# Optimization experiments

Hardware: AMD Instinct MI355X
Metric: run time of the kernel (lower is better)

## Reference

```python
import jax, jax.numpy as jnp
from jax import lax
import numpy as np

D = 1024      # input_size
H = D // 2    # proj hidden
T = 25        # num_ner_labels
B, S = 64, 512


def setup_inputs() -> dict:
    key = jax.random.key(0)
    ks = jax.random.split(key, 8)
    sc1 = 1.0 / np.sqrt(D)
    sc2 = 1.0 / np.sqrt(H)
    return {
        "encoder_out": jax.random.normal(ks[0], (B, S, D), dtype=jnp.float32),
        "W1": jax.random.uniform(ks[1], (D, H), jnp.float32, -sc1, sc1),
        "b1": jax.random.uniform(ks[2], (H,), jnp.float32, -sc1, sc1),
        "W2": jax.random.uniform(ks[3], (H, T), jnp.float32, -sc2, sc2),
        "b2": jax.random.uniform(ks[4], (T,), jnp.float32, -sc2, sc2),
        "start_trans": jax.random.uniform(ks[5], (T,), jnp.float32, -0.1, 0.1),
        "end_trans": jax.random.uniform(ks[6], (T,), jnp.float32, -0.1, 0.1),
        "trans": jax.random.uniform(ks[7], (T, T), jnp.float32, -0.1, 0.1),
        "ner_labels": jax.random.randint(jax.random.fold_in(key, 1), (B, S), 0, T, dtype=jnp.int64),
        "mask": jnp.ones((B, S), dtype=bool),
    }


def _crf_nll(emissions, start_trans, end_trans, trans, labels, mask):
    # torchcrf negative mean log-likelihood, batch_first
    maskf = mask.astype(emissions.dtype)
    # numerator: score of gold path
    em_at_tag = jnp.take_along_axis(emissions, labels[..., None], axis=2)[..., 0]  # [B,S]
    score0 = start_trans[labels[:, 0]] + em_at_tag[:, 0]
    trans_sc = trans[labels[:, :-1], labels[:, 1:]]                                # [B,S-1]
    step_score = (trans_sc + em_at_tag[:, 1:]) * maskf[:, 1:]
    last_idx = mask.sum(axis=1).astype(jnp.int32) - 1
    last_tag = jnp.take_along_axis(labels, last_idx[:, None].astype(labels.dtype), axis=1)[:, 0]
    numerator = score0 + step_score.sum(axis=1) + end_trans[last_tag]
    # denominator: log partition via forward algorithm (scan over time)
    alpha0 = start_trans[None, :] + emissions[:, 0]                                # [B,T]
    em_rest = jnp.swapaxes(emissions[:, 1:], 0, 1)                                 # [S-1,B,T]
    m_rest = jnp.swapaxes(mask[:, 1:], 0, 1)                                       # [S-1,B]

    def step(alpha, xs):
        em_t, m_t = xs
        new = jax.scipy.special.logsumexp(
            alpha[:, :, None] + trans[None, :, :] + em_t[:, None, :], axis=1)
        return jnp.where(m_t[:, None], new, alpha), None

    alpha, _ = lax.scan(step, alpha0, (em_rest, m_rest))
    log_Z = jax.scipy.special.logsumexp(alpha + end_trans[None, :], axis=1)        # [B]
    return -jnp.mean(numerator - log_Z)


def reference(encoder_out, W1, b1, W2, b2, start_trans, end_trans, trans, ner_labels, mask):
    h = jax.nn.gelu(encoder_out @ W1 + b1, approximate=False)  # dropout is eval-mode identity
    emissions = h @ W2 + b2                                    # [B,S,T]
    return _crf_nll(emissions, start_trans, end_trans, trans, ner_labels, mask)
```

## Files before the change

### kernel.cpp

```cpp
#include <hip/hip_runtime.h>
#include <math.h>

#define DD 1024
#define HH 512
#define TT 25
#define BB 64
#define SS 512
#define MM (BB*SS)
#define NC 32

typedef __attribute__((ext_vector_type(8))) short short8;
typedef __attribute__((ext_vector_type(4))) float floatx4;
typedef __attribute__((ext_vector_type(16))) float floatx16;

static __device__ __forceinline__ unsigned short f2bf(float f) {
  unsigned u = __float_as_uint(f);
  u = (u + 0x7FFFu + ((u >> 16) & 1u)) >> 16;
  return (unsigned short)u;
}
static __device__ __forceinline__ float bf2f(unsigned short s) {
  return __uint_as_float(((unsigned)s) << 16);
}
static __device__ __forceinline__ float rl(float v, int i) {
  return __int_as_float(__builtin_amdgcn_readlane(__float_as_int(v), i));
}
static __device__ __forceinline__ void load_lds16(const void* g, void* l) {
  __builtin_amdgcn_global_load_lds(
      (const __attribute__((address_space(1))) unsigned int*)g,
      (__attribute__((address_space(3))) unsigned int*)l, 16, 0, 0);
}
union U4S8 { uint4 u; short8 s; };

__global__ __launch_bounds__(256) void k_prep(
    const float* __restrict__ W1, const float* __restrict__ W2,
    unsigned short* __restrict__ W1T2, unsigned short* __restrict__ W2p) {
  const int t = threadIdx.x;
  if (blockIdx.y < 8) {
    __shared__ unsigned short tile[64 * 72];
    const int k0 = blockIdx.x * 64, n0 = blockIdx.y * 64;
    #pragma unroll
    for (int it = 0; it < 16; it++) {
      int idx = t + it * 256;
      int kk = idx >> 6, nn = idx & 63;
      tile[nn * 72 + kk] = f2bf(W1[(size_t)(k0 + kk) * HH + n0 + nn]);
    }
    __syncthreads();
    #pragma unroll
    for (int it = 0; it < 4; it++) {
      int idx = (t + it * 256) * 4;
      int nn = idx >> 6, kk = idx & 63;
      ushort4 v;
      v.x = tile[nn * 72 + kk];     v.y = tile[nn * 72 + kk + 1];
      v.z = tile[nn * 72 + kk + 2]; v.w = tile[nn * 72 + kk + 3];
      int kt = (k0 >> 5) + (kk >> 5), kkk = kk & 31;
      *(ushort4*)(W1T2 + (size_t)kt * (HH * 32) + (n0 + nn) * 32 + kkk) = v;
    }
  } else {
    #pragma unroll
    for (int e = 0; e < 4; e++) {
      int idx = blockIdx.x * 1024 + t + e * 256;
      int row = idx >> 9, k = idx & 511;
      float v = (row < TT) ? W2[(size_t)k * TT + row] : 0.f;
      W2p[(size_t)row * HH + k] = f2bf(v);
    }
  }
}

__global__ __launch_bounds__(256, 4) void k_emis(
    const float* __restrict__ X, const unsigned short* __restrict__ W1T2,
    const float* __restrict__ b1, const unsigned short* __restrict__ W2p,
    const float* __restrict__ b2, float* __restrict__ em) {
  __shared__ short lds[12544];
  short* sX  = lds;
  short* sBt = lds + 2048;

  const int tid  = threadIdx.x;
  const int lane = tid & 63;
  const int w    = tid >> 6;
  const int l15  = lane & 15;
  const int kc   = lane >> 4;
  const int m0   = blockIdx.x * 64;
  const int colbase = blockIdx.y * 256;

  floatx4 acc[4][4];
  #pragma unroll
  for (int a = 0; a < 4; a++)
    #pragma unroll
    for (int b = 0; b < 4; b++)
      acc[a][b] = (floatx4){0.f, 0.f, 0.f, 0.f};

  const int am = tid >> 2;
  const int ac = tid & 3;
  const float* Xrow = X + (size_t)(m0 + am) * DD + ac * 8;

  const unsigned short* gW = W1T2 + (size_t)(colbase + w * 64) * 32 + lane * 8;
  short* lW = sBt + w * 64 * 32;

  float4 xv0 = *(const float4*)(Xrow);
  float4 xv1 = *(const float4*)(Xrow + 4);

  for (int k0 = 0; k0 < DD; k0 += 32) {
    __syncthreads();
    const unsigned short* g = gW + (size_t)(k0 >> 5) * (HH * 32);
    #pragma unroll
    for (int j = 0; j < 4; j++)
      load_lds16(g + j * 512, lW + j * 512);
    unsigned p0 = (unsigned)f2bf(xv0.x) | ((unsigned)f2bf(xv0.y) << 16);
    unsigned p1 = (unsigned)f2bf(xv0.z) | ((unsigned)f2bf(xv0.w) << 16);
    unsigned p2 = (unsigned)f2bf(xv1.x) | ((unsigned)f2bf(xv1.y) << 16);
    unsigned p3 = (unsigned)f2bf(xv1.z) | ((unsigned)f2bf(xv1.w) << 16);
    *(uint4*)(sX + am * 32 + ac * 8) = make_uint4(p0, p1, p2, p3);
    if (k0 + 32 < DD) {
      xv0 = *(const float4*)(Xrow + k0 + 32);
      xv1 = *(const float4*)(Xrow + k0 + 36);
    }
    __syncthreads();
    short8 af[4], bfr[4];
    #pragma unroll
    for (int mt = 0; mt < 4; mt++)
      af[mt] = *(const short8*)(sX + (mt * 16 + l15) * 32 + kc * 8);
    #pragma unroll
    for (int nt = 0; nt < 4; nt++)
      bfr[nt] = *(const short8*)(sBt + (w * 64 + nt * 16 + l15) * 32 + kc * 8);
    #pragma unroll
    for (int mt = 0; mt < 4; mt++)
      #pragma unroll
      for (int nt = 0; nt < 4; nt++)
        acc[mt][nt] = __builtin_amdgcn_mfma_f32_16x16x32_bf16(af[mt], bfr[nt], acc[mt][nt], 0, 0, 0);
  }

  short* sH = lds;
  float* sC = (float*)(lds + 8448);
  const int mt_g = w & 1, kh_g = w >> 1;

  short8 w2f[2][4];
  #pragma unroll
  for (int nt2 = 0; nt2 < 2; nt2++)
    #pragma unroll
    for (int ks = 0; ks < 4; ks++)
      w2f[nt2][ks] = *(const short8*)(W2p + (size_t)(nt2 * 16 + l15) * HH
                                      + colbase + kh_g * 128 + ks * 32 + kc * 8);

  #pragma unroll
  for (int half = 0; half < 2; half++) {
    __syncthreads();
    #pragma unroll
    for (int mt2 = 0; mt2 < 2; mt2++) {
      int mt = half * 2 + mt2;
      #pragma unroll
      for (int nt = 0; nt < 4; nt++) {
        int n = w * 64 + nt * 16 + l15;
        float bias = b1[colbase + n];
        #pragma unroll
        for (int r = 0; r < 4; r++) {
          int ml = mt2 * 16 + kc * 4 + r;
          float v = acc[mt][nt][r] + bias;
          float g = 0.5f * v * (1.0f + erff(v * 0.70710678118654752f));
          sH[ml * 264 + n] = (short)f2bf(g);
        }
      }
    }
    __syncthreads();
    #pragma unroll
    for (int nt2 = 0; nt2 < 2; nt2++) {
      floatx4 c2 = (floatx4){0.f, 0.f, 0.f, 0.f};
      #pragma unroll
      for (int ks = 0; ks < 4; ks++) {
        short8 a2 = *(const short8*)(sH + (mt_g * 16 + l15) * 264 + kh_g * 128 + ks * 32 + kc * 8);
        c2 = __builtin_amdgcn_mfma_f32_16x16x32_bf16(a2, w2f[nt2][ks], c2, 0, 0, 0);
      }
      #pragma unroll
      for (int r = 0; r < 4; r++)
        sC[kh_g * 1024 + (mt_g * 16 + kc * 4 + r) * 32 + nt2 * 16 + l15] = c2[r];
    }
    __syncthreads();
    for (int o = tid; o < 32 * TT; o += 256) {
      int m = o / TT, t = o % TT;
      float val = sC[m * 32 + t] + sC[1024 + m * 32 + t];
      if (blockIdx.y == 0) val += b2[t];
      atomicAdd(em + (size_t)(m0 + half * 32 + m) * TT + t, val);
    }
  }
}

__global__ __launch_bounds__(64) void k_chunk(
    const float* __restrict__ em, const float* __restrict__ trans,
    float* __restrict__ Mats) {
  const int b = blockIdx.x, c = blockIdx.y;
  const int lane = threadIdx.x;
  const int h = lane >> 5;
  const int n = lane & 31;
  const float* emb = em + (size_t)b * SS * TT;

  unsigned a1p[4], a2p[4];
  #pragma unroll
  for (int p = 0; p < 4; p++) {
    int i0 = h * 8 + 2 * p, i1 = i0 + 1;
    unsigned lo = (n < TT && i0 < TT) ? (unsigned)f2bf(__expf(trans[i0 * TT + n])) : 0u;
    unsigned hi = (n < TT && i1 < TT) ? (unsigned)f2bf(__expf(trans[i1 * TT + n])) : 0u;
    a1p[p] = lo | (hi << 16);
    int j0 = 16 + h * 8 + 2 * p, j1 = j0 + 1;
    lo = (n < TT && j0 < TT) ? (unsigned)f2bf(__expf(trans[j0 * TT + n])) : 0u;
    hi = (n < TT && j1 < TT) ? (unsigned)f2bf(__expf(trans[j1 * TT + n])) : 0u;
    a2p[p] = lo | (hi << 16);
  }
  U4S8 A1, A2;
  A1.u = make_uint4(a1p[0], a1p[1], a1p[2], a1p[3]);
  A2.u = make_uint4(a2p[0], a2p[1], a2p[2], a2p[3]);

  unsigned bp1[4], bp2[4];
  #pragma unroll
  for (int p = 0; p < 4; p++) {
    int k0 = h * 8 + 2 * p;
    bp1[p] = ((k0 == n) ? 0x3F80u : 0u) | ((k0 + 1 == n) ? 0x3F800000u : 0u);
    int k2 = 16 + h * 8 + 2 * p;
    bp2[p] = ((k2 == n) ? 0x3F80u : 0u) | ((k2 + 1 == n) ? 0x3F800000u : 0u);
  }

  const int s0 = 1 + c * 16;
  const int nst = (s0 + 16 <= SS) ? 16 : (SS - s0);

  float emv[16], f[16];
  #pragma unroll
  for (int e = 0; e < 16; e++) {
    int r = (e & 3) + 8 * (e >> 2) + 4 * h;
    emv[e] = (r < TT) ? emb[s0 * TT + r] : 0.f;
  }

  for (int t = 0; t < nst; t++) {
    const float rs = (t == 8) ? 32.0f : 0.0f;
    float ex[16];
    #pragma unroll
    for (int e = 0; e < 16; e++) ex[e] = __expf(emv[e] - rs);
    int sn = (s0 + t + 1 < SS) ? s0 + t + 1 : SS - 1;
    #pragma unroll
    for (int e = 0; e < 16; e++) {
      int r = (e & 3) + 8 * (e >> 2) + 4 * h;
      emv[e] = (r < TT) ? emb[sn * TT + r] : 0.f;
    }
    U4S8 B1, B2;
    B1.u = make_uint4(bp1[0], bp1[1], bp1[2], bp1[3]);
    B2.u = make_uint4(bp2[0], bp2[1], bp2[2], bp2[3]);
    floatx16 D = __builtin_amdgcn_mfma_f32_32x32x16_bf16(A1.s, B1.s,
                   __builtin_amdgcn_mfma_f32_32x32x16_bf16(A2.s, B2.s,
                     (floatx16){0.f,0.f,0.f,0.f,0.f,0.f,0.f,0.f,
                                0.f,0.f,0.f,0.f,0.f,0.f,0.f,0.f}, 0,0,0), 0,0,0);
    #pragma unroll
    for (int e = 0; e < 16; e++) f[e] = D[e] * ex[e];
    if (t == nst - 1) break;
    unsigned P[16];
    #pragma unroll
    for (int p = 0; p < 8; p++)
      P[p] = (unsigned)f2bf(f[2 * p]) | ((unsigned)f2bf(f[2 * p + 1]) << 16);
    unsigned sp[8];
    #pragma unroll
    for (int p = 0; p < 8; p++)
      sp[p] = (unsigned)__shfl_xor((int)P[p], 32);
    bool up = (h == 1);
    bp1[0] = up ? sp[2] : P[0];
    bp1[1] = up ? sp[3] : P[1];
    bp1[2] = up ? P[2] : sp[0];
    bp1[3] = up ? P[3] : sp[1];
    bp2[0] = up ? sp[6] : P[4];
    bp2[1] = up ? sp[7] : P[5];
    bp2[2] = up ? P[6] : sp[4];
    bp2[3] = up ? P[7] : sp[5];
  }

  if (n < TT) {
    float* Mc = Mats + ((size_t)(b * NC + c)) * (TT * TT) + n * TT;
    #pragma unroll
    for (int e = 0; e < 16; e++) {
      int r = (e & 3) + 8 * (e >> 2) + 4 * h;
      if (r < TT) Mc[r] = __logf(f[e]) + 32.0f;
    }
  }
}

__global__ __launch_bounds__(64) void k_comb(
    const float* __restrict__ em, const float* __restrict__ start,
    const float* __restrict__ endt, const float* __restrict__ trans,
    const int* __restrict__ labels, const float* __restrict__ Mats,
    float* __restrict__ partial) {
  const int b = blockIdx.x;
  const int tid = threadIdx.x;
  const float* emb = em + (size_t)b * SS * TT;
  const int* lab = labels + b * SS;

  float part = 0.f;
  for (int s = tid; s < SS; s += 64) {
    int l = lab[s];
    if (s == 0) part += start[l] + emb[l];
    else        part += trans[lab[s - 1] * TT + l] + emb[s * TT + l];
  }
  #pragma unroll
  for (int off = 32; off; off >>= 1) part += __shfl_xor(part, off);
  float num = part + endt[lab[SS - 1]];

  const int jj = (tid < TT) ? tid : 0;
  float a = (tid < TT) ? start[tid] + emb[tid] : -1e30f;
  const float* Mb = Mats + (size_t)b * NC * (TT * TT);
  for (int c = 0; c < NC; c++) {
    const float* Mc = Mb + c * (TT * TT);
    float col[TT];
    float mxc = -1e30f;
    #pragma unroll
    for (int i = 0; i < TT; i++) {
      col[i] = Mc[i * TT + jj];
      mxc = fmaxf(mxc, col[i]);
    }
    float a0 = __builtin_amdgcn_readfirstlane(a);
    float p = __expf(a - a0);
    float d0 = 0.f, d1 = 0.f, d2 = 0.f, d3 = 0.f;
    #pragma unroll
    for (int i = 0; i < 24; i += 4) {
      d0 = fmaf(rl(p, i + 0), __expf(col[i + 0] - mxc), d0);
      d1 = fmaf(rl(p, i + 1), __expf(col[i + 1] - mxc), d1);
      d2 = fmaf(rl(p, i + 2), __expf(col[i + 2] - mxc), d2);
      d3 = fmaf(rl(p, i + 3), __expf(col[i + 3] - mxc), d3);
    }
    d0 = fmaf(rl(p, 24), __expf(col[24] - mxc), d0);
    float anew = a0 + mxc + __logf((d0 + d1) + (d2 + d3));
    a = (tid < TT) ? anew : -1e30f;
  }

  float v = (tid < TT) ? a + endt[tid] : -1e30f;
  float mx = v;
  #pragma unroll
  for (int off = 16; off; off >>= 1) mx = fmaxf(mx, __shfl_xor(mx, off, 32));
  float e = (tid < TT) ? __expf(v - mx) : 0.f;
  #pragma unroll
  for (int off = 16; off; off >>= 1) e += __shfl_xor(e, off, 32);
  if (tid == 0) partial[b] = (mx + __logf(e)) - num;
}

__global__ void k_final(const float* __restrict__ partial, float* __restrict__ out) {
  int tid = threadIdx.x;
  float v = partial[tid];
  #pragma unroll
  for (int off = 32; off; off >>= 1) v += __shfl_xor(v, off);
  if (tid == 0) out[0] = v * (1.0f / 64.0f);
}

extern "C" void kernel_launch(void* const* d_in, const int* in_sizes, int n_in,
                              void* d_out, int out_size, void* d_ws, size_t ws_size,
                              hipStream_t stream) {
  const float* X   = (const float*)d_in[0];
  const float* W1  = (const float*)d_in[1];
  const float* b1  = (const float*)d_in[2];
  const float* W2  = (const float*)d_in[3];
  const float* b2  = (const float*)d_in[4];
  const float* st  = (const float*)d_in[5];
  const float* en  = (const float*)d_in[6];
  const float* tr  = (const float*)d_in[7];
  const int* labels = (const int*)d_in[8];

  char* ws = (char*)d_ws;
  unsigned short* W1T2 = (unsigned short*)ws;
  unsigned short* W2p  = (unsigned short*)(ws + 0x100000);
  float* em            = (float*)(ws + 0x110000);
  float* Mats          = (float*)(ws + 0x430000);
  float* partial       = (float*)(ws + 0x930000);

  k_prep <<<dim3(16, 9), 256, 0, stream>>>(W1, W2, W1T2, W2p);
  hipMemsetAsync(em, 0, (size_t)MM * TT * sizeof(float), stream);
  k_emis <<<dim3(512, 2), 256, 0, stream>>>(X, W1T2, b1, W2p, b2, em);
  k_chunk<<<dim3(BB, NC), 64, 0, stream>>>(em, tr, Mats);
  k_comb <<<BB, 64, 0, stream>>>(em, st, en, tr, labels, Mats, partial);
  k_final<<<1, 64, 0, stream>>>(partial, (float*)d_out);
}
```

Measured before the change: 306.2 us.

## Double-buffer LDS tiles in emission GEMM K-loop with one barrier per step

Converts the k_emis K-loop to a double-buffered LDS scheme. The next W1 tile is issued via async global-to-LDS loads and the next X tile is converted to bf16 and written into the alternate buffer while MFMAs run on the current one. This halves the barriers per iteration and hides load latency behind compute. The larger LDS footprint and an extra register stage lower the launch-bounds occupancy target from 4 to 3 blocks per CU.

```diff
diff --git a/kernel.cpp b/kernel.cpp
--- a/kernel.cpp
+++ b/kernel.cpp
@@ -66,13 +66,11 @@
   }
 }
 
-__global__ __launch_bounds__(256, 4) void k_emis(
+__global__ __launch_bounds__(256, 3) void k_emis(
     const float* __restrict__ X, const unsigned short* __restrict__ W1T2,
     const float* __restrict__ b1, const unsigned short* __restrict__ W2p,
     const float* __restrict__ b2, float* __restrict__ em) {
-  __shared__ short lds[12544];
-  short* sX  = lds;
-  short* sBt = lds + 2048;
+  __shared__ __attribute__((aligned(16))) short lds[20480];
 
   const int tid  = threadIdx.x;
   const int lane = tid & 63;
@@ -94,39 +92,66 @@
   const float* Xrow = X + (size_t)(m0 + am) * DD + ac * 8;
 
   const unsigned short* gW = W1T2 + (size_t)(colbase + w * 64) * 32 + lane * 8;
-  short* lW = sBt + w * 64 * 32;
-
-  float4 xv0 = *(const float4*)(Xrow);
-  float4 xv1 = *(const float4*)(Xrow + 4);
-
-  for (int k0 = 0; k0 < DD; k0 += 32) {
-    __syncthreads();
-    const unsigned short* g = gW + (size_t)(k0 >> 5) * (HH * 32);
-    #pragma unroll
-    for (int j = 0; j < 4; j++)
-      load_lds16(g + j * 512, lW + j * 512);
+
+  {
+    float4 xv0 = *(const float4*)(Xrow);
+    float4 xv1 = *(const float4*)(Xrow + 4);
     unsigned p0 = (unsigned)f2bf(xv0.x) | ((unsigned)f2bf(xv0.y) << 16);
     unsigned p1 = (unsigned)f2bf(xv0.z) | ((unsigned)f2bf(xv0.w) << 16);
     unsigned p2 = (unsigned)f2bf(xv1.x) | ((unsigned)f2bf(xv1.y) << 16);
     unsigned p3 = (unsigned)f2bf(xv1.z) | ((unsigned)f2bf(xv1.w) << 16);
-    *(uint4*)(sX + am * 32 + ac * 8) = make_uint4(p0, p1, p2, p3);
-    if (k0 + 32 < DD) {
-      xv0 = *(const float4*)(Xrow + k0 + 32);
-      xv1 = *(const float4*)(Xrow + k0 + 36);
-    }
-    __syncthreads();
+    *(uint4*)(lds + am * 32 + ac * 8) = make_uint4(p0, p1, p2, p3);
+  }
+  {
+    short* lW = lds + 4096 + w * 2048;
+    #pragma unroll
+    for (int j = 0; j < 4; j++)
+      load_lds16(gW + j * 512, lW + j * 512);
+  }
+  float4 yv0 = *(const float4*)(Xrow + 32);
+  float4 yv1 = *(const float4*)(Xrow + 36);
+  __syncthreads();
+
+  for (int t = 0; t < 32; ++t) {
+    const int cur = t & 1, nxt = cur ^ 1;
+    short* sXc = lds + cur * 2048;
+    short* sBc = lds + 4096 + cur * 8192;
+
+    float4 zv0, zv1;
+    if (t < 31) {
+      const unsigned short* g = gW + (size_t)(t + 1) * (HH * 32);
+      short* lW = lds + 4096 + nxt * 8192 + w * 2048;
+      #pragma unroll
+      for (int j = 0; j < 4; j++)
+        load_lds16(g + j * 512, lW + j * 512);
+      if (t < 30) {
+        zv0 = *(const float4*)(Xrow + (t + 2) * 32);
+        zv1 = *(const float4*)(Xrow + (t + 2) * 32 + 4);
+      }
+    }
+
     short8 af[4], bfr[4];
     #pragma unroll
     for (int mt = 0; mt < 4; mt++)
-      af[mt] = *(const short8*)(sX + (mt * 16 + l15) * 32 + kc * 8);
+      af[mt] = *(const short8*)(sXc + (mt * 16 + l15) * 32 + kc * 8);
     #pragma unroll
     for (int nt = 0; nt < 4; nt++)
-      bfr[nt] = *(const short8*)(sBt + (w * 64 + nt * 16 + l15) * 32 + kc * 8);
+      bfr[nt] = *(const short8*)(sBc + (w * 64 + nt * 16 + l15) * 32 + kc * 8);
     #pragma unroll
     for (int mt = 0; mt < 4; mt++)
       #pragma unroll
       for (int nt = 0; nt < 4; nt++)
         acc[mt][nt] = __builtin_amdgcn_mfma_f32_16x16x32_bf16(af[mt], bfr[nt], acc[mt][nt], 0, 0, 0);
+
+    if (t < 31) {
+      unsigned p0 = (unsigned)f2bf(yv0.x) | ((unsigned)f2bf(yv0.y) << 16);
+      unsigned p1 = (unsigned)f2bf(yv0.z) | ((unsigned)f2bf(yv0.w) << 16);
+      unsigned p2 = (unsigned)f2bf(yv1.x) | ((unsigned)f2bf(yv1.y) << 16);
+      unsigned p3 = (unsigned)f2bf(yv1.z) | ((unsigned)f2bf(yv1.w) << 16);
+      *(uint4*)(lds + nxt * 2048 + am * 32 + ac * 8) = make_uint4(p0, p1, p2, p3);
+      if (t < 30) { yv0 = zv0; yv1 = zv1; }
+    }
+    __syncthreads();
   }
 
   short* sH = lds;
```

New measurement: 335.2 us. +9.5%, slower.
